# Kernel tuning notes

Hardware: AMD Instinct MI355X
Metric: run time of the kernel (lower is better)

## Reference

```python
import jax, jax.numpy as jnp
import numpy as np

CHUNK = 16  # chunksize from init


def setup_inputs() -> dict:
    key = jax.random.key(0)
    k0, k1, k2, k3 = jax.random.split(key, 4)
    B, C, L = 8, 512, 8192
    x = jax.random.normal(k0, (B, C, L), jnp.float32)
    # per-channel EMA decay, uniform in [0, r_max=0.9)
    gamma = jax.random.uniform(k1, (C,), jnp.float32) * 0.9
    # 1x1 conv weights: Conv1d(dim, dim//8, 1) and Conv1d(dim//8, dim, 1)
    w1 = jax.random.normal(k2, (C // 8, C), jnp.float32) / np.sqrt(C)
    b1 = jnp.zeros((C // 8,), jnp.float32)
    w2 = jax.random.normal(k3, (C, C // 8), jnp.float32) / np.sqrt(C // 8)
    b2 = jnp.zeros((C,), jnp.float32)
    return {"x": x, "gamma": gamma, "w1": w1, "b1": b1, "w2": w2, "b2": b2}


def reference(x, gamma, w1, b1, w2, b2):
    # x: [B, C, L]
    B, C, L = x.shape
    cs = CHUNK
    pad = (-L) % cs
    xp = jnp.pad(x, ((0, 0), (0, 0), (0, pad)))
    N = xp.shape[2] // cs
    # chunked average pooling -> [B, C, N]   (q() fake-quant is identity in fp)
    xc = xp.reshape(B, C, N, cs).mean(axis=3)

    # causal EMA recurrence over chunk steps: y_t = g*y_{t-1} + (1-g)*x_t
    def step(y, xt):
        y = gamma * y + (1.0 - gamma) * xt  # [B, C]
        return y, y

    xcn = jnp.moveaxis(xc, 2, 0)  # [N, B, C]
    _, ys = jax.lax.scan(step, jnp.zeros((B, C), x.dtype), xcn)
    e = jnp.transpose(ys, (1, 2, 0))  # [B, C, N]

    # SE bottleneck: 1x1 conv -> ReLU -> 1x1 conv
    h = jax.nn.relu(jnp.einsum('oc,bcn->bon', w1, e) + b1[:, None])  # [B, C//8, N]
    o = jnp.einsum('co,bon->bcn', w2, h) + b2[:, None]               # [B, C, N]
    gate = jax.nn.sigmoid(o)

    # expand gate back to per-timestep and apply to residual
    gate = jnp.repeat(gate, cs, axis=2)[:, :, :L]
    return gate * x
```

## Files before the change

kernel.cpp:

```cpp
#include <hip/hip_runtime.h>
#include <math.h>

#define B 8
#define C 512
#define L 8192
#define CS 16
#define N 512
#define C8 64
#define SEG 16
#define SL 32
#define ROWS 4096

__global__ __launch_bounds__(256) void pool_k(const float* __restrict__ x,
                                              float* __restrict__ pool) {
    __shared__ float tile[16][17];
    const int t = threadIdx.x;
    const int bid = blockIdx.x;
    const int nt = bid & 31;
    const int ct = (bid >> 5) & 31;
    const int b  = bid >> 10;
    const int w    = t >> 6;
    const int lane = t & 63;

#pragma unroll
    for (int i = 0; i < 4; ++i) {
        const int c_local = i * 4 + w;
        const int c = ct * 16 + c_local;
        const float4 v = reinterpret_cast<const float4*>(x)[
            (size_t)(b * C + c) * (L / 4) + nt * 64 + lane];
        float s = v.x + v.y + v.z + v.w;
        s += __shfl_down(s, 1, 4);
        s += __shfl_down(s, 2, 4);
        if ((lane & 3) == 0)
            tile[c_local][lane >> 2] = s * (1.0f / 16.0f);
    }
    __syncthreads();

    const int n_local = t >> 4;
    const int c_local = t & 15;
    pool[(size_t)(b * N + nt * 16 + n_local) * C + ct * 16 + c_local] =
        tile[c_local][n_local];
}

__global__ __launch_bounds__(256) void emaA_k(const float* __restrict__ gamma,
                                              const float* __restrict__ pool,
                                              float* __restrict__ carry,
                                              const float* __restrict__ w1,
                                              const float* __restrict__ w2,
                                              float* __restrict__ w1t4,
                                              float* __restrict__ w2t4) {
    const int id = blockIdx.x * 256 + threadIdx.x;
    if (id < C8 * C) {
        {
            const int o = id >> 9;
            const int k = id & (C - 1);
            w1t4[((k >> 2) * C8 + o) * 4 + (k & 3)] = w1[id];
        }
        {
            const int c = id >> 6;
            const int k = id & (C8 - 1);
            w2t4[((k >> 2) * C + c) * 4 + (k & 3)] = w2[id];
        }
    }
    const int c = id & (C - 1);
    const int rest = id >> 9;
    const int s = rest & (SEG - 1);
    const int b = rest >> 4;
    const float g = gamma[c];
    const float omg = 1.0f - g;
    const float* p = pool + ((size_t)(b * N + s * SL)) * C + c;
    float y = 0.0f;
#pragma unroll 8
    for (int i = 0; i < SL; ++i)
        y = fmaf(g, y, omg * p[(size_t)i * C]);
    carry[(size_t)(b * SEG + s) * C + c] = y;
}

__global__ __launch_bounds__(256) void se1_k(const float* __restrict__ pool,
                                             const float* __restrict__ carry,
                                             const float* __restrict__ gamma,
                                             const float* __restrict__ w1t4,
                                             float* __restrict__ ph) {
    __shared__ float e_s[32 * 256];
    const int t = threadIdx.x;
    const int rb = blockIdx.x >> 1;
    const int ks = blockIdx.x & 1;
    const int b = rb >> 4;
    const int s = rb & 15;
    const int row0 = rb * 32;

#pragma unroll
    for (int i = 0; i < 8; ++i) {
        const int idx = i * 256 + t;
        const int r = idx >> 6;
        const int kk = idx & 63;
        reinterpret_cast<float4*>(e_s)[idx] =
            reinterpret_cast<const float4*>(pool + (size_t)(row0 + r) * C + ks * 256)[kk];
    }
    __syncthreads();

    {
        const int c = ks * 256 + t;
        const float g = gamma[c];
        const float omg = 1.0f - g;
        float g32 = g * g;
        g32 *= g32; g32 *= g32; g32 *= g32; g32 *= g32;
        float E = 0.0f;
        const float* cb = carry + (size_t)b * SEG * C + c;
        for (int tt = 0; tt < s; ++tt)
            E = fmaf(g32, E, cb[(size_t)tt * C]);
        float y = E;
#pragma unroll
        for (int r = 0; r < 32; ++r) {
            y = fmaf(g, y, omg * e_s[r * 256 + t]);
            e_s[r * 256 + t] = y;
        }
    }
    __syncthreads();

    const int oc = t & 31;
    const int jg = t >> 5;
    float a0[4] = {0.f, 0.f, 0.f, 0.f};
    float a1[4] = {0.f, 0.f, 0.f, 0.f};
    const float4* w1v = reinterpret_cast<const float4*>(w1t4);
    const float4* es4 = reinterpret_cast<const float4*>(e_s);
#pragma unroll 4
    for (int k4 = 0; k4 < 64; ++k4) {
        const float4 wa = w1v[(size_t)(ks * 64 + k4) * C8 + oc];
        const float4 wb = w1v[(size_t)(ks * 64 + k4) * C8 + oc + 32];
#pragma unroll
        for (int r = 0; r < 4; ++r) {
            const float4 ev = es4[(jg * 4 + r) * 64 + k4];
            a0[r] = fmaf(wa.x, ev.x, a0[r]); a0[r] = fmaf(wa.y, ev.y, a0[r]);
            a0[r] = fmaf(wa.z, ev.z, a0[r]); a0[r] = fmaf(wa.w, ev.w, a0[r]);
            a1[r] = fmaf(wb.x, ev.x, a1[r]); a1[r] = fmaf(wb.y, ev.y, a1[r]);
            a1[r] = fmaf(wb.z, ev.z, a1[r]); a1[r] = fmaf(wb.w, ev.w, a1[r]);
        }
    }
    float* pbase = ph + ((size_t)ks * ROWS + row0) * C8;
#pragma unroll
    for (int r = 0; r < 4; ++r) {
        pbase[(size_t)(jg * 4 + r) * C8 + oc]      = a0[r];
        pbase[(size_t)(jg * 4 + r) * C8 + oc + 32] = a1[r];
    }
}

__global__ __launch_bounds__(256) void se2_k(const float* __restrict__ ph,
                                             const float* __restrict__ b1,
                                             const float* __restrict__ w2t4,
                                             const float* __restrict__ b2,
                                             float* __restrict__ gate) {
    __shared__ float h_s[32 * C8];
    const int t = threadIdx.x;
    const int rb = blockIdx.x >> 2;
    const int ct = blockIdx.x & 3;
    const int row0 = rb * 32;
    const int b = rb >> 4;
    const int n0 = (rb & 15) * 32;

    {
        const float4* p0 = reinterpret_cast<const float4*>(ph + (size_t)row0 * C8);
        const float4* p1 = reinterpret_cast<const float4*>(ph + (size_t)(ROWS + row0) * C8);
        const float4* b1v = reinterpret_cast<const float4*>(b1);
#pragma unroll
        for (int i = 0; i < 2; ++i) {
            const int idx = i * 256 + t;
            const float4 u = p0[idx];
            const float4 v = p1[idx];
            const float4 bb = b1v[idx & 15];
            float4 hv;
            hv.x = fmaxf(bb.x + u.x + v.x, 0.f);
            hv.y = fmaxf(bb.y + u.y + v.y, 0.f);
            hv.z = fmaxf(bb.z + u.z + v.z, 0.f);
            hv.w = fmaxf(bb.w + u.w + v.w, 0.f);
            reinterpret_cast<float4*>(h_s)[idx] = hv;
        }
    }
    __syncthreads();

    const int cl = t & 63;
    const int jg = t >> 6;
    const int c = ct * 128 + cl;
    float acc0[8], acc1[8];
    const float bb0 = b2[c];
    const float bb1 = b2[c + 64];
#pragma unroll
    for (int j = 0; j < 8; ++j) { acc0[j] = bb0; acc1[j] = bb1; }
    const float4* w2v = reinterpret_cast<const float4*>(w2t4);
    const float4* hs4 = reinterpret_cast<const float4*>(h_s);
#pragma unroll
    for (int k4 = 0; k4 < 16; ++k4) {
        const float4 wa = w2v[(size_t)k4 * C + c];
        const float4 wb = w2v[(size_t)k4 * C + c + 64];
#pragma unroll
        for (int j = 0; j < 8; ++j) {
            const float4 hv = hs4[(jg * 8 + j) * 16 + k4];
            acc0[j] = fmaf(wa.x, hv.x, acc0[j]); acc0[j] = fmaf(wa.y, hv.y, acc0[j]);
            acc0[j] = fmaf(wa.z, hv.z, acc0[j]); acc0[j] = fmaf(wa.w, hv.w, acc0[j]);
            acc1[j] = fmaf(wb.x, hv.x, acc1[j]); acc1[j] = fmaf(wb.y, hv.y, acc1[j]);
            acc1[j] = fmaf(wb.z, hv.z, acc1[j]); acc1[j] = fmaf(wb.w, hv.w, acc1[j]);
        }
    }
    {
        float4 o0, o1;
        float* g0 = gate + ((size_t)(b * C + c)) * N + n0 + jg * 8;
        float* g1 = gate + ((size_t)(b * C + c + 64)) * N + n0 + jg * 8;
        o0.x = 1.0f / (1.0f + __expf(-acc0[0]));
        o0.y = 1.0f / (1.0f + __expf(-acc0[1]));
        o0.z = 1.0f / (1.0f + __expf(-acc0[2]));
        o0.w = 1.0f / (1.0f + __expf(-acc0[3]));
        o1.x = 1.0f / (1.0f + __expf(-acc0[4]));
        o1.y = 1.0f / (1.0f + __expf(-acc0[5]));
        o1.z = 1.0f / (1.0f + __expf(-acc0[6]));
        o1.w = 1.0f / (1.0f + __expf(-acc0[7]));
        reinterpret_cast<float4*>(g0)[0] = o0;
        reinterpret_cast<float4*>(g0)[1] = o1;
        o0.x = 1.0f / (1.0f + __expf(-acc1[0]));
        o0.y = 1.0f / (1.0f + __expf(-acc1[1]));
        o0.z = 1.0f / (1.0f + __expf(-acc1[2]));
        o0.w = 1.0f / (1.0f + __expf(-acc1[3]));
        o1.x = 1.0f / (1.0f + __expf(-acc1[4]));
        o1.y = 1.0f / (1.0f + __expf(-acc1[5]));
        o1.z = 1.0f / (1.0f + __expf(-acc1[6]));
        o1.w = 1.0f / (1.0f + __expf(-acc1[7]));
        reinterpret_cast<float4*>(g1)[0] = o0;
        reinterpret_cast<float4*>(g1)[1] = o1;
    }
}

__global__ __launch_bounds__(256) void apply_k(const float* __restrict__ x,
                                               const float* __restrict__ gate,
                                               float* __restrict__ out) {
    const size_t id = (size_t)blockIdx.x * 256 + threadIdx.x;
    const int per_row = L / 4;
    const int bc = (int)(id / per_row);
    const int wi = (int)(id % per_row);
    const int n = wi >> 2;

    const float g = gate[(size_t)bc * N + n];
    float4 v = reinterpret_cast<const float4*>(x)[id];
    v.x *= g; v.y *= g; v.z *= g; v.w *= g;
    reinterpret_cast<float4*>(out)[id] = v;
}

extern "C" void kernel_launch(void* const* d_in, const int* in_sizes, int n_in,
                              void* d_out, int out_size, void* d_ws, size_t ws_size,
                              hipStream_t stream) {
    const float* x     = (const float*)d_in[0];
    const float* gamma = (const float*)d_in[1];
    const float* w1    = (const float*)d_in[2];
    const float* b1    = (const float*)d_in[3];
    const float* w2    = (const float*)d_in[4];
    const float* b2    = (const float*)d_in[5];
    float* out = (float*)d_out;

    char* ws = (char*)d_ws;
    size_t off = 0;
    float* pool  = (float*)(ws + off); off += (size_t)B * N * C * 4;
    float* gate  = (float*)(ws + off); off += (size_t)B * N * C * 4;
    float* w1t4  = (float*)(ws + off); off += (size_t)C8 * C * 4;
    float* w2t4  = (float*)(ws + off); off += (size_t)C8 * C * 4;
    float* carry = (float*)(ws + off); off += (size_t)B * SEG * C * 4;
    float* ph    = (float*)(ws + off); off += (size_t)2 * ROWS * C8 * 4;

    pool_k<<<B * 32 * 32, 256, 0, stream>>>(x, pool);
    emaA_k<<<(B * SEG * C) / 256, 256, 0, stream>>>(gamma, pool, carry, w1, w2, w1t4, w2t4);
    se1_k<<<128 * 2, 256, 0, stream>>>(pool, carry, gamma, w1t4, ph);
    se2_k<<<128 * 4, 256, 0, stream>>>(ph, b1, w2t4, b2, gate);
    apply_k<<<(B * C * L / 4) / 256, 256, 0, stream>>>(x, gate, out);
}
```

Before: 96.91 us.

## Fuse chunk pooling and EMA scan into one per-channel-tile kernel

Replaces the separate pooling kernel, the segment-carry EMA kernel and the in-se1 EMA fixup with one kernel. Each block owns 8 channels of one batch across the whole sequence: it pools into shared memory, runs a two-level scan (per-segment carries, then a serial prefix with gamma^16), and writes the finished EMA output. This removes a launch, the pool round-trip through global memory and the carry buffer, and it drops the recurrence work from se1. In exchange the grid shrinks from 8192 to 512 blocks, each streaming 256KB of x, which may leave less memory-level parallelism for the bandwidth-bound pooling read.

```diff
diff --git a/kernel.cpp b/kernel.cpp
--- a/kernel.cpp
+++ b/kernel.cpp
@@ -7,86 +7,103 @@
 #define CS 16
 #define N 512
 #define C8 64
-#define SEG 16
-#define SL 32
 #define ROWS 4096
-
-__global__ __launch_bounds__(256) void pool_k(const float* __restrict__ x,
-                                              float* __restrict__ pool) {
-    __shared__ float tile[16][17];
+#define CTILE 8
+
+__global__ __launch_bounds__(256) void pool_ema_k(
+    const float* __restrict__ x, const float* __restrict__ gamma,
+    float* __restrict__ e,
+    const float* __restrict__ w1, const float* __restrict__ w2,
+    float* __restrict__ w1t4, float* __restrict__ w2t4) {
+    __shared__ float cm[CTILE * 545];
+    __shared__ float carry_s[CTILE][32];
+    __shared__ float pre_s[CTILE][32];
     const int t = threadIdx.x;
     const int bid = blockIdx.x;
-    const int nt = bid & 31;
-    const int ct = (bid >> 5) & 31;
-    const int b  = bid >> 10;
-    const int w    = t >> 6;
-    const int lane = t & 63;
-
-#pragma unroll
-    for (int i = 0; i < 4; ++i) {
-        const int c_local = i * 4 + w;
-        const int c = ct * 16 + c_local;
-        const float4 v = reinterpret_cast<const float4*>(x)[
-            (size_t)(b * C + c) * (L / 4) + nt * 64 + lane];
-        float s = v.x + v.y + v.z + v.w;
-        s += __shfl_down(s, 1, 4);
-        s += __shfl_down(s, 2, 4);
-        if ((lane & 3) == 0)
-            tile[c_local][lane >> 2] = s * (1.0f / 16.0f);
-    }
-    __syncthreads();
-
-    const int n_local = t >> 4;
-    const int c_local = t & 15;
-    pool[(size_t)(b * N + nt * 16 + n_local) * C + ct * 16 + c_local] =
-        tile[c_local][n_local];
-}
-
-__global__ __launch_bounds__(256) void emaA_k(const float* __restrict__ gamma,
-                                              const float* __restrict__ pool,
-                                              float* __restrict__ carry,
-                                              const float* __restrict__ w1,
-                                              const float* __restrict__ w2,
-                                              float* __restrict__ w1t4,
-                                              float* __restrict__ w2t4) {
-    const int id = blockIdx.x * 256 + threadIdx.x;
-    if (id < C8 * C) {
-        {
-            const int o = id >> 9;
-            const int k = id & (C - 1);
-            w1t4[((k >> 2) * C8 + o) * 4 + (k & 3)] = w1[id];
-        }
-        {
-            const int c = id >> 6;
-            const int k = id & (C8 - 1);
-            w2t4[((k >> 2) * C + c) * 4 + (k & 3)] = w2[id];
-        }
-    }
-    const int c = id & (C - 1);
-    const int rest = id >> 9;
-    const int s = rest & (SEG - 1);
-    const int b = rest >> 4;
-    const float g = gamma[c];
+    const int ct = bid & 63;
+    const int b = bid >> 6;
+
+    const int gid = bid * 256 + t;
+    if (gid < C8 * C) {
+        const int o = gid >> 9, k = gid & (C - 1);
+        w1t4[((k >> 2) * C8 + o) * 4 + (k & 3)] = w1[gid];
+        const int c2 = gid >> 6, k2 = gid & (C8 - 1);
+        w2t4[((k2 >> 2) * C + c2) * 4 + (k2 & 3)] = w2[gid];
+    }
+
+    const int w = t >> 6, lane = t & 63;
+#pragma unroll
+    for (int cr = 0; cr < 2; ++cr) {
+        const int cl = w + 4 * cr;
+        const size_t row4 = (size_t)(b * C + ct * CTILE + cl) * (L / 4);
+#pragma unroll
+        for (int r = 0; r < 4; ++r) {
+            float4 f[8];
+#pragma unroll
+            for (int u = 0; u < 8; ++u)
+                f[u] = reinterpret_cast<const float4*>(x)[row4 + r * 512 + u * 64 + lane];
+#pragma unroll
+            for (int u = 0; u < 8; ++u) {
+                float s = f[u].x + f[u].y + f[u].z + f[u].w;
+                s += __shfl_down(s, 1, 4);
+                s += __shfl_down(s, 2, 4);
+                if ((lane & 3) == 0) {
+                    const int chunk = r * 128 + u * 16 + (lane >> 2);
+                    cm[cl * 545 + (chunk >> 4) * 17 + (chunk & 15)] = s * (1.0f / 16.0f);
+                }
+            }
+        }
+    }
+    __syncthreads();
+
+    const int cl = t >> 5, s = t & 31;
+    const float g = gamma[ct * CTILE + cl];
     const float omg = 1.0f - g;
-    const float* p = pool + ((size_t)(b * N + s * SL)) * C + c;
-    float y = 0.0f;
-#pragma unroll 8
-    for (int i = 0; i < SL; ++i)
-        y = fmaf(g, y, omg * p[(size_t)i * C]);
-    carry[(size_t)(b * SEG + s) * C + c] = y;
-}
-
-__global__ __launch_bounds__(256) void se1_k(const float* __restrict__ pool,
-                                             const float* __restrict__ carry,
-                                             const float* __restrict__ gamma,
+    {
+        float y = 0.0f;
+#pragma unroll
+        for (int i = 0; i < 16; ++i)
+            y = fmaf(g, y, omg * cm[cl * 545 + s * 17 + i]);
+        carry_s[cl][s] = y;
+    }
+    __syncthreads();
+    if (t < CTILE) {
+        const float gg = gamma[ct * CTILE + t];
+        float g16 = gg * gg; g16 *= g16; g16 *= g16; g16 *= g16;
+        float E = 0.0f;
+#pragma unroll
+        for (int ss = 0; ss < 32; ++ss) {
+            pre_s[t][ss] = E;
+            E = fmaf(g16, E, carry_s[t][ss]);
+        }
+    }
+    __syncthreads();
+    {
+        float y = pre_s[cl][s];
+#pragma unroll
+        for (int i = 0; i < 16; ++i) {
+            y = fmaf(g, y, omg * cm[cl * 545 + s * 17 + i]);
+            cm[cl * 545 + s * 17 + i] = y;
+        }
+    }
+    __syncthreads();
+
+    float* ebase = e + (size_t)b * N * C + ct * CTILE;
+#pragma unroll
+    for (int r = 0; r < 16; ++r) {
+        const int idx = r * 256 + t;
+        const int n = idx >> 3, c2 = idx & 7;
+        ebase[(size_t)n * C + c2] = cm[c2 * 545 + (n >> 4) * 17 + (n & 15)];
+    }
+}
+
+__global__ __launch_bounds__(256) void se1_k(const float* __restrict__ e,
                                              const float* __restrict__ w1t4,
                                              float* __restrict__ ph) {
     __shared__ float e_s[32 * 256];
     const int t = threadIdx.x;
     const int rb = blockIdx.x >> 1;
     const int ks = blockIdx.x & 1;
-    const int b = rb >> 4;
-    const int s = rb & 15;
     const int row0 = rb * 32;
 
 #pragma unroll
@@ -95,26 +112,7 @@
         const int r = idx >> 6;
         const int kk = idx & 63;
         reinterpret_cast<float4*>(e_s)[idx] =
-            reinterpret_cast<const float4*>(pool + (size_t)(row0 + r) * C + ks * 256)[kk];
-    }
-    __syncthreads();
-
-    {
-        const int c = ks * 256 + t;
-        const float g = gamma[c];
-        const float omg = 1.0f - g;
-        float g32 = g * g;
-        g32 *= g32; g32 *= g32; g32 *= g32; g32 *= g32;
-        float E = 0.0f;
-        const float* cb = carry + (size_t)b * SEG * C + c;
-        for (int tt = 0; tt < s; ++tt)
-            E = fmaf(g32, E, cb[(size_t)tt * C]);
-        float y = E;
-#pragma unroll
-        for (int r = 0; r < 32; ++r) {
-            y = fmaf(g, y, omg * e_s[r * 256 + t]);
-            e_s[r * 256 + t] = y;
-        }
+            reinterpret_cast<const float4*>(e + (size_t)(row0 + r) * C + ks * 256)[kk];
     }
     __syncthreads();
 
@@ -256,16 +254,14 @@
 
     char* ws = (char*)d_ws;
     size_t off = 0;
-    float* pool  = (float*)(ws + off); off += (size_t)B * N * C * 4;
+    float* e     = (float*)(ws + off); off += (size_t)B * N * C * 4;
     float* gate  = (float*)(ws + off); off += (size_t)B * N * C * 4;
     float* w1t4  = (float*)(ws + off); off += (size_t)C8 * C * 4;
     float* w2t4  = (float*)(ws + off); off += (size_t)C8 * C * 4;
-    float* carry = (float*)(ws + off); off += (size_t)B * SEG * C * 4;
     float* ph    = (float*)(ws + off); off += (size_t)2 * ROWS * C8 * 4;
 
-    pool_k<<<B * 32 * 32, 256, 0, stream>>>(x, pool);
-    emaA_k<<<(B * SEG * C) / 256, 256, 0, stream>>>(gamma, pool, carry, w1, w2, w1t4, w2t4);
-    se1_k<<<128 * 2, 256, 0, stream>>>(pool, carry, gamma, w1t4, ph);
+    pool_ema_k<<<B * 64, 256, 0, stream>>>(x, gamma, e, w1, w2, w1t4, w2t4);
+    se1_k<<<128 * 2, 256, 0, stream>>>(e, w1t4, ph);
     se2_k<<<128 * 4, 256, 0, stream>>>(ph, b1, w2t4, b2, gate);
     apply_k<<<(B * C * L / 4) / 256, 256, 0, stream>>>(x, gate, out);
 }
```

Measured after the change: 95.26 us. About the same (-1.7%).
